# Kernel tuning notes

Measured on AMD Instinct MI355X. Metric: run time of the kernel, lower is better.

Reference implementation:

```python
import jax, jax.numpy as jnp
import numpy as np

N_NODES = 50000
N_EDGES = 600000
D = 128
EPS = 1e-5
AVG_D_LOG = float(np.log(4 + 1))  # avg_d={'log': log(avg_d+1)}, avg_d=4


def setup_inputs() -> dict:
    key = jax.random.key(0)
    ks = jax.random.split(key, 8)
    h = jax.random.normal(ks[0], (N_NODES, D), dtype=jnp.float32)
    # guarantee every node has at least one incoming edge (self-loop)
    edge_dst = jnp.concatenate([
        jnp.arange(N_NODES, dtype=jnp.int64),
        jax.random.randint(ks[1], (N_EDGES - N_NODES,), 0, N_NODES).astype(jnp.int64),
    ])
    edge_src = jax.random.randint(ks[2], (N_EDGES,), 0, N_NODES).astype(jnp.int64)
    def lin(k, fan_in, fan_out):
        lim = 1.0 / np.sqrt(fan_in)
        return jax.random.uniform(k, (fan_in, fan_out), jnp.float32, -lim, lim)
    W_pre = lin(ks[3], 2 * D, D)
    b_pre = jnp.zeros((D,), jnp.float32)
    W_post = lin(ks[4], 12 * D + D, D)  # 4 aggregators * 3 scalers * D + in_dim
    b_post = jnp.zeros((D,), jnp.float32)
    W_mix = lin(ks[5], D, D)
    b_mix = jnp.zeros((D,), jnp.float32)
    return {"h": h, "edge_src": edge_src, "edge_dst": edge_dst,
            "W_pre": W_pre, "b_pre": b_pre, "W_post": W_post,
            "b_post": b_post, "W_mix": W_mix, "b_mix": b_mix}


def reference(h, edge_src, edge_dst, W_pre, b_pre, W_post, b_post, W_mix, b_mix):
    n = h.shape[0]
    # pretrans_edges: cat(src, dst) -> Linear -> ReLU (MLP act) -> ReLU (outer)
    z2 = jnp.concatenate([h[edge_src], h[edge_dst]], axis=1)        # [E, 2D]
    e = jax.nn.relu(z2 @ W_pre + b_pre)                             # [E, D]
    # multi-aggregator segment reduce over destination nodes
    deg = jax.ops.segment_sum(jnp.ones_like(edge_dst, jnp.float32), edge_dst, n)  # [N]
    inv_deg = 1.0 / deg[:, None]
    mean = jax.ops.segment_sum(e, edge_dst, n) * inv_deg
    mean_sq = jax.ops.segment_sum(e * e, edge_dst, n) * inv_deg
    std = jnp.sqrt(jax.nn.relu(mean_sq - mean * mean) + EPS)
    mx = jax.ops.segment_max(e, edge_dst, n)
    mn = jax.ops.segment_min(e, edge_dst, n)
    agg = jnp.concatenate([mean, mx, mn, std], axis=1)              # [N, 4D]
    # scalers: identity, amplification, attenuation
    log_d = jnp.log(deg + 1.0)[:, None]
    scaled = jnp.concatenate([agg, agg * (log_d / AVG_D_LOG), agg * (AVG_D_LOG / log_d)], axis=1)  # [N, 12D]
    # posttrans: cat(h, aggregated) -> Linear -> ReLU
    hp = jax.nn.relu(jnp.concatenate([h, scaled], axis=1) @ W_post + b_post)  # [N, D]
    # mixing network + residual (node_dim == out_dim)
    out = h + jax.nn.leaky_relu(hp @ W_mix + b_mix, negative_slope=0.01)
    return out
```

## Files before the change

### kernel.cpp

```cpp
#include <hip/hip_runtime.h>
#include <hip/hip_bf16.h>

#define N_NODES 50000
#define N_EDGES 600000
#define D 128
#define NB_SCAN 196

constexpr float AVG_D_LOG = 1.6094379124341003f;
constexpr float EPS_V = 1e-5f;

#define PQ_B     0ul
#define AGG_B    25600000ul
#define HBF_B    76800000ul
#define WPRET2_B 89600000ul
#define WPOSTT_B 89665536ul
#define WMIXT_B  90091520ul
#define DEGC_B   90124288ul
#define OFF_B    90324288ul
#define CUR_B    90524352ul
#define SRCS_B   90724352ul
#define BSUM_B   93124352ul

typedef __attribute__((ext_vector_type(8))) short bf16x8;
typedef __attribute__((ext_vector_type(4))) float f32x4;

__device__ __forceinline__ short f2b(float f) {
    unsigned u = __builtin_bit_cast(unsigned, f);
    u += 0x7fffu + ((u >> 16) & 1u);
    return (short)(u >> 16);
}
__device__ __forceinline__ unsigned pk2(float a, float b) {
    return (unsigned)(unsigned short)f2b(a) | ((unsigned)(unsigned short)f2b(b) << 16);
}
__device__ __forceinline__ float blo(unsigned u) { return __uint_as_float(u << 16); }
__device__ __forceinline__ float bhi(unsigned u) { return __uint_as_float(u & 0xffff0000u); }

__device__ __forceinline__ void gld_lds16(const void* g, void* l) {
    __builtin_amdgcn_global_load_lds(
        (const __attribute__((address_space(1))) void*)g,
        (__attribute__((address_space(3))) void*)l, 16, 0, 0);
}

#define WAIT_BAR(N) do {                                              \
    asm volatile("s_waitcnt vmcnt(" #N ")" ::: "memory");             \
    __builtin_amdgcn_sched_barrier(0);                                \
    __builtin_amdgcn_s_barrier();                                     \
    __builtin_amdgcn_sched_barrier(0);                                \
} while (0)
#define BAR_ONLY() do {                                               \
    __builtin_amdgcn_sched_barrier(0);                                \
    __builtin_amdgcn_s_barrier();                                     \
    __builtin_amdgcn_sched_barrier(0);                                \
} while (0)

__global__ __launch_bounds__(256) void prep_kernel(
    const float* __restrict__ h, const float* __restrict__ Wpre,
    const float* __restrict__ Wpost, const float* __restrict__ Wmix,
    short* __restrict__ hbf, short* __restrict__ wpreT2,
    short* __restrict__ wpostT, short* __restrict__ wmixT,
    int* __restrict__ degc, int* __restrict__ cursor)
{
    long i = (long)blockIdx.x * 256 + threadIdx.x;
    if (i < 800000) {
        float4 a = *(const float4*)(h + i * 8);
        float4 b = *(const float4*)(h + i * 8 + 4);
        int4 v;
        v.x = (int)pk2(a.x, a.y); v.y = (int)pk2(a.z, a.w);
        v.z = (int)pk2(b.x, b.y); v.w = (int)pk2(b.z, b.w);
        *(int4*)(hbf + i * 8) = v;
        return;
    }
    i -= 800000;
    if (i < 32768) {
        int n = i >> 7, k = i & 127;
        float v = (n < 128) ? Wpre[k * 128 + n] : Wpre[(k + 128) * 128 + (n - 128)];
        wpreT2[n * 128 + k] = f2b(v);
        return;
    }
    i -= 32768;
    if (i < 212992) { int k = i >> 7, n = i & 127; wpostT[n * 1664 + k] = f2b(Wpost[k * 128 + n]); return; }
    i -= 212992;
    if (i < 16384) { int k = i >> 7, n = i & 127; wmixT[n * 128 + k] = f2b(Wmix[k * 128 + n]); return; }
    i -= 16384;
    if (i < N_NODES) { degc[i] = 0; return; }
    i -= N_NODES;
    if (i < N_NODES) cursor[i] = 0;
}
#define PREP_BLOCKS ((800000 + 32768 + 212992 + 16384 + 2 * N_NODES + 255) / 256)

__global__ __launch_bounds__(256) void hist_kernel(const int* __restrict__ edst, int* __restrict__ degc) {
    int e = blockIdx.x * 256 + threadIdx.x;
    if (e < N_EDGES) atomicAdd(&degc[edst[e]], 1);
}

__global__ __launch_bounds__(256) void scan1_kernel(const int* __restrict__ degc, int* __restrict__ bsum) {
    int n = blockIdx.x * 256 + threadIdx.x;
    int v = (n < N_NODES) ? degc[n] : 0;
#pragma unroll
    for (int o = 32; o > 0; o >>= 1) v += __shfl_down(v, o);
    __shared__ int w4[4];
    if ((threadIdx.x & 63) == 0) w4[threadIdx.x >> 6] = v;
    __syncthreads();
    if (threadIdx.x == 0) bsum[blockIdx.x] = w4[0] + w4[1] + w4[2] + w4[3];
}

__global__ __launch_bounds__(256) void scan2_kernel(int* __restrict__ bsum, int* __restrict__ off) {
    __shared__ int sd[256];
    int tid = threadIdx.x;
    int v = (tid < NB_SCAN) ? bsum[tid] : 0;
    sd[tid] = v;
    __syncthreads();
    for (int o = 1; o < 256; o <<= 1) {
        int t = (tid >= o) ? sd[tid - o] : 0;
        __syncthreads();
        sd[tid] += t;
        __syncthreads();
    }
    if (tid < NB_SCAN) bsum[tid] = sd[tid] - v;
    if (tid == 0) off[N_NODES] = sd[255];
}

__global__ __launch_bounds__(256) void scan3_kernel(const int* __restrict__ degc,
                                                    const int* __restrict__ bsum, int* __restrict__ off) {
    __shared__ int sd[256];
    int tid = threadIdx.x;
    int n = blockIdx.x * 256 + tid;
    int v = (n < N_NODES) ? degc[n] : 0;
    sd[tid] = v;
    __syncthreads();
    for (int o = 1; o < 256; o <<= 1) {
        int t = (tid >= o) ? sd[tid - o] : 0;
        __syncthreads();
        sd[tid] += t;
        __syncthreads();
    }
    if (n < N_NODES) off[n] = sd[tid] - v + bsum[blockIdx.x];
}

__global__ __launch_bounds__(256) void scatter_kernel(const int* __restrict__ esrc, const int* __restrict__ edst,
                                                      const int* __restrict__ off, int* __restrict__ cursor,
                                                      int* __restrict__ srcs) {
    int e = blockIdx.x * 256 + threadIdx.x;
    if (e < N_EDGES) {
        int d = edst[e];
        int p = off[d] + atomicAdd(&cursor[d], 1);
        srcs[p] = esrc[e];
    }
}

__global__ __launch_bounds__(256) void gemm_pq_kernel(
    const short* __restrict__ hbf, const short* __restrict__ wpreT2,
    const float* __restrict__ bpre, short* __restrict__ PQ)
{
    __shared__ __align__(16) short As[128][72];
    __shared__ __align__(16) short Bs[128][72];

    const int tid = threadIdx.x;
    const int cg = blockIdx.x & 1;
    const int bn = (blockIdx.x >> 1) * 128;
    const int lane = tid & 63, wv = tid >> 6;
    const int lm = lane & 15, quad = lane >> 4;

    f32x4 acc[2][8];
#pragma unroll
    for (int a = 0; a < 2; a++)
#pragma unroll
        for (int b = 0; b < 8; b++) acc[a][b] = (f32x4){0.f, 0.f, 0.f, 0.f};

#pragma unroll
    for (int kc = 0; kc < 2; kc++) {
        __syncthreads();
#pragma unroll
        for (int t = 0; t < 4; t++) {
            int q = tid + t * 256;
            int m = q >> 3, seg = q & 7;
            int n = bn + m; if (n >= N_NODES) n = N_NODES - 1;
            *(int4*)&As[m][seg * 8] = *(const int4*)(hbf + (long)n * 128 + kc * 64 + seg * 8);
        }
#pragma unroll
        for (int t = 0; t < 4; t++) {
            int q = tid + t * 256;
            int n = q >> 3, seg = q & 7;
            *(int4*)&Bs[n][seg * 8] = *(const int4*)(wpreT2 + (cg * 128 + n) * 128 + kc * 64 + seg * 8);
        }
        __syncthreads();
#pragma unroll
        for (int ks = 0; ks < 2; ks++) {
            const int ko = ks * 32 + quad * 8;
            bf16x8 a0 = *(const bf16x8*)&As[wv * 32 + lm][ko];
            bf16x8 a1 = *(const bf16x8*)&As[wv * 32 + 16 + lm][ko];
#pragma unroll
            for (int ct = 0; ct < 8; ct++) {
                bf16x8 b = *(const bf16x8*)&Bs[ct * 16 + lm][ko];
                acc[0][ct] = __builtin_amdgcn_mfma_f32_16x16x32_bf16(b, a0, acc[0][ct], 0, 0, 0);
                acc[1][ct] = __builtin_amdgcn_mfma_f32_16x16x32_bf16(b, a1, acc[1][ct], 0, 0, 0);
            }
        }
    }

#pragma unroll
    for (int rt = 0; rt < 2; rt++) {
        int row = wv * 32 + rt * 16 + lm;
        int n = bn + row;
        if (n >= N_NODES) continue;
        short* dst = PQ + (long)n * 256;
#pragma unroll
        for (int ct = 0; ct < 8; ct++) {
            int col = cg * 128 + ct * 16 + quad * 4;
            float v0 = acc[rt][ct][0], v1 = acc[rt][ct][1], v2 = acc[rt][ct][2], v3 = acc[rt][ct][3];
            if (cg) {
                float4 bv = *(const float4*)(bpre + (col - 128));
                v0 += bv.x; v1 += bv.y; v2 += bv.z; v3 += bv.w;
            }
            int2 pkd; pkd.x = (int)pk2(v0, v1); pkd.y = (int)pk2(v2, v3);
            *(int2*)(dst + col) = pkd;
        }
    }
}

__global__ __launch_bounds__(256) void edgestats_kernel(
    const short* __restrict__ PQ, const int* __restrict__ srcs,
    const int* __restrict__ off, short* __restrict__ aggbf)
{
    const int wv = threadIdx.x >> 6, lane = threadIdx.x & 63;
    const int n = blockIdx.x * 4 + wv;
    const unsigned* Pb = (const unsigned*)PQ;

    const int s0 = __builtin_amdgcn_readfirstlane(off[n]);
    const int s1 = __builtin_amdgcn_readfirstlane(off[n + 1]);

    unsigned qu = Pb[(long)n * 128 + 64 + lane];
    const float qa = blo(qu), qb = bhi(qu);

    float sA = 0.f, sB = 0.f, qA = 0.f, qB = 0.f;
    float mxA = -1e30f, mxB = -1e30f, mnA = 1e30f, mnB = 1e30f;

    int p = s0;
    for (; p + 8 <= s1; p += 8) {
        int idx[8];
#pragma unroll
        for (int j = 0; j < 8; j++) idx[j] = srcs[p + j];
        unsigned u[8];
#pragma unroll
        for (int j = 0; j < 8; j++) u[j] = Pb[(long)idx[j] * 128 + lane];
#pragma unroll
        for (int j = 0; j < 8; j++) {
            float a = blo(u[j]) + qa; a = a > 0.f ? a : 0.f;
            float b = bhi(u[j]) + qb; b = b > 0.f ? b : 0.f;
            sA += a; sB += b; qA += a * a; qB += b * b;
            mxA = fmaxf(mxA, a); mxB = fmaxf(mxB, b);
            mnA = fminf(mnA, a); mnB = fminf(mnB, b);
        }
    }
    for (; p < s1; p++) {
        unsigned u = Pb[(long)srcs[p] * 128 + lane];
        float a = blo(u) + qa; a = a > 0.f ? a : 0.f;
        float b = bhi(u) + qb; b = b > 0.f ? b : 0.f;
        sA += a; sB += b; qA += a * a; qB += b * b;
        mxA = fmaxf(mxA, a); mxB = fmaxf(mxB, b);
        mnA = fminf(mnA, a); mnB = fminf(mnB, b);
    }

    float inv = 1.0f / (float)(s1 - s0);
    float mA = sA * inv, mB = sB * inv;
    float vA = qA * inv - mA * mA; vA = vA > 0.f ? vA : 0.f;
    float vB = qB * inv - mB * mB; vB = vB > 0.f ? vB : 0.f;
    float stA = sqrtf(vA + EPS_V), stB = sqrtf(vB + EPS_V);

    unsigned* ag = (unsigned*)(aggbf + (long)n * 512);
    ag[lane]       = pk2(mA, mB);
    ag[64 + lane]  = pk2(mxA, mxB);
    ag[128 + lane] = pk2(mnA, mnB);
    ag[192 + lane] = pk2(stA, stB);
}


__device__ __forceinline__ void stageA_t(short* ldsT, const short* src, int rs, int co,
                                         int bn, int wv, int lane) {
    const int sub = lane >> 3, seg = lane & 7;
    const int sg = (seg ^ sub) * 8;
#pragma unroll
    for (int t = 0; t < 4; t++) {
        int i = wv * 4 + t;
        int row = i * 8 + sub;
        int n = bn + row; if (n >= N_NODES) n = N_NODES - 1;
        gld_lds16(src + (long)n * rs + co + sg, ldsT + i * 512);
    }
}
__device__ __forceinline__ void stageB_t(short* ldsT, const short* src, int rs, int co,
                                         int wv, int lane) {
    const int sub = lane >> 3, seg = lane & 7;
    const int sg = (seg ^ sub) * 8;
#pragma unroll
    for (int t = 0; t < 4; t++) {
        int i = wv * 4 + t;
        int row = i * 8 + sub;
        gld_lds16(src + (long)row * rs + co + sg, ldsT + i * 512);
    }
}

#define MFMA_ITER(AB, BB, ACC)                                                      \
    {                                                                               \
        _Pragma("unroll")                                                           \
        for (int ks = 0; ks < 2; ks++) {                                            \
            const int qx = (((ks * 4 + quad) ^ r7) * 8);                            \
            bf16x8 a0 = *(const bf16x8*)&(AB)[(wv * 32 + lm) * 64 + qx];            \
            bf16x8 a1 = *(const bf16x8*)&(AB)[(wv * 32 + 16 + lm) * 64 + qx];       \
            _Pragma("unroll")                                                       \
            for (int ct = 0; ct < 8; ct++) {                                        \
                bf16x8 b = *(const bf16x8*)&(BB)[(ct * 16 + lm) * 64 + qx];         \
                ACC[0][ct] = __builtin_amdgcn_mfma_f32_16x16x32_bf16(b, a0, ACC[0][ct], 0, 0, 0); \
                ACC[1][ct] = __builtin_amdgcn_mfma_f32_16x16x32_bf16(b, a1, ACC[1][ct], 0, 0, 0); \
            }                                                                       \
        }                                                                           \
    }

__global__ __launch_bounds__(256, 2) void node_kernel(
    const float* __restrict__ h, const short* __restrict__ hbf, const short* __restrict__ aggbf,
    const int* __restrict__ degc, const short* __restrict__ wpostT, const float* __restrict__ bpost,
    const short* __restrict__ wmixT, const float* __restrict__ bmix, float* __restrict__ out)
{
    __shared__ __align__(16) short As[2][8192];
    __shared__ __align__(16) short Bs[2][8192];
    __shared__ float sAmp[128], sAtt[128];

    const int tid = threadIdx.x;
    const int bn = blockIdx.x * 128;
    const int lane = tid & 63, wv = tid >> 6;
    const int lm = lane & 15, quad = lane >> 4;
    const int r7 = lm & 7;

    if (tid < 128) {
        int n = bn + tid; if (n >= N_NODES) n = N_NODES - 1;
        float d = (float)degc[n];
        float ld = logf(d + 1.0f);
        sAmp[tid] = ld * (1.0f / AVG_D_LOG);
        sAtt[tid] = AVG_D_LOG / ld;
    }
    __syncthreads();

    f32x4 accI[2][8], accM[2][8], accT[2][8];
#pragma unroll
    for (int a = 0; a < 2; a++)
#pragma unroll
        for (int b = 0; b < 8; b++) {
            accI[a][b] = (f32x4){0.f, 0.f, 0.f, 0.f};
            accM[a][b] = (f32x4){0.f, 0.f, 0.f, 0.f};
            accT[a][b] = (f32x4){0.f, 0.f, 0.f, 0.f};
        }


    stageA_t(As[0], hbf, 128, 0, bn, wv, lane);
    stageB_t(Bs[0], wpostT, 1664, 0, wv, lane);

    stageA_t(As[1], hbf, 128, 64, bn, wv, lane);
    stageB_t(Bs[1], wpostT, 1664, 64, wv, lane);
    WAIT_BAR(8);
    MFMA_ITER(As[0], Bs[0], accI);
    BAR_ONLY();

    stageB_t(Bs[0], wpostT, 1664, 2 * 64, wv, lane);
    stageA_t(As[0], aggbf, 512, 0, bn, wv, lane);
    WAIT_BAR(8);
    MFMA_ITER(As[1], Bs[1], accI);
    BAR_ONLY();

    int pb = 0;
    for (int j = 0; j < 8; j++) {
        short* Ac = As[j & 1];
        stageB_t(Bs[pb ^ 1], wpostT, 1664, (10 + j) * 64, wv, lane);
        if (j < 7) {
            int jn = j + 1;
            stageA_t(As[jn & 1], aggbf, 512, (jn >> 1) * 128 + (jn & 1) * 64, bn, wv, lane);
            WAIT_BAR(8);
        } else {
            WAIT_BAR(4);
        }
        MFMA_ITER(Ac, Bs[pb], accI);
        BAR_ONLY();

        stageB_t(Bs[pb], wpostT, 1664, (18 + j) * 64, wv, lane);
        if (j < 7) { WAIT_BAR(8); } else { WAIT_BAR(4); }
        MFMA_ITER(Ac, Bs[pb ^ 1], accM);
        BAR_ONLY();

        if (j < 7) stageB_t(Bs[pb ^ 1], wpostT, 1664, (3 + j) * 64, wv, lane);
        else       stageB_t(Bs[pb ^ 1], wmixT, 128, 0, wv, lane);
        WAIT_BAR(4);
        MFMA_ITER(Ac, Bs[pb], accT);
        BAR_ONLY();
        pb ^= 1;
    }

    stageB_t(Bs[1], wmixT, 128, 64, wv, lane);

    const float am0 = sAmp[wv * 32 + lm],      at0 = sAtt[wv * 32 + lm];
    const float am1 = sAmp[wv * 32 + 16 + lm], at1 = sAtt[wv * 32 + 16 + lm];
#pragma unroll
    for (int rt = 0; rt < 2; rt++) {
        const float am = rt ? am1 : am0, at = rt ? at1 : at0;
        const int row = wv * 32 + rt * 16 + lm;
#pragma unroll
        for (int ct = 0; ct < 8; ct++) {
            float4 bv = *(const float4*)(bpost + ct * 16 + quad * 4);
            float v0 = accI[rt][ct][0] + am * accM[rt][ct][0] + at * accT[rt][ct][0] + bv.x;
            float v1 = accI[rt][ct][1] + am * accM[rt][ct][1] + at * accT[rt][ct][1] + bv.y;
            float v2 = accI[rt][ct][2] + am * accM[rt][ct][2] + at * accT[rt][ct][2] + bv.z;
            float v3 = accI[rt][ct][3] + am * accM[rt][ct][3] + at * accT[rt][ct][3] + bv.w;
            v0 = v0 > 0.f ? v0 : 0.f; v1 = v1 > 0.f ? v1 : 0.f;
            v2 = v2 > 0.f ? v2 : 0.f; v3 = v3 > 0.f ? v3 : 0.f;
            int2 pkd; pkd.x = (int)pk2(v0, v1); pkd.y = (int)pk2(v2, v3);
            const int cb = (ct & 3) * 32 + quad * 8;
            const int sb = ((((cb >> 4) ^ r7) << 4) | (cb & 15));
            *(int2*)((char*)As[ct >> 2] + row * 128 + sb) = pkd;
        }
    }
    __syncthreads();

    f32x4 accO[2][8];
#pragma unroll
    for (int a = 0; a < 2; a++)
#pragma unroll
        for (int b = 0; b < 8; b++) accO[a][b] = (f32x4){0.f, 0.f, 0.f, 0.f};
#pragma unroll
    for (int kc = 0; kc < 2; kc++) {
        MFMA_ITER(As[kc], Bs[kc], accO);
    }

#pragma unroll
    for (int rt = 0; rt < 2; rt++) {
        int row = wv * 32 + rt * 16 + lm;
        int n = bn + row;
        if (n >= N_NODES) continue;
#pragma unroll
        for (int ct = 0; ct < 8; ct++) {
            int col = ct * 16 + quad * 4;
            float4 bv = *(const float4*)(bmix + col);
            float4 hv = *(const float4*)(h + (long)n * 128 + col);
            float4 o;
            float v0 = accO[rt][ct][0] + bv.x; v0 = v0 > 0.f ? v0 : 0.01f * v0; o.x = hv.x + v0;
            float v1 = accO[rt][ct][1] + bv.y; v1 = v1 > 0.f ? v1 : 0.01f * v1; o.y = hv.y + v1;
            float v2 = accO[rt][ct][2] + bv.z; v2 = v2 > 0.f ? v2 : 0.01f * v2; o.z = hv.z + v2;
            float v3 = accO[rt][ct][3] + bv.w; v3 = v3 > 0.f ? v3 : 0.01f * v3; o.w = hv.w + v3;
            *(float4*)(out + (long)n * 128 + col) = o;
        }
    }
}

extern "C" void kernel_launch(void* const* d_in, const int* in_sizes, int n_in,
                              void* d_out, int out_size, void* d_ws, size_t ws_size,
                              hipStream_t stream) {
    const float* h     = (const float*)d_in[0];
    const int*   esrc  = (const int*)d_in[1];
    const int*   edst  = (const int*)d_in[2];
    const float* Wpre  = (const float*)d_in[3];
    const float* bpre  = (const float*)d_in[4];
    const float* Wpost = (const float*)d_in[5];
    const float* bpost = (const float*)d_in[6];
    const float* Wmix  = (const float*)d_in[7];
    const float* bmix  = (const float*)d_in[8];
    float* out = (float*)d_out;
    char* ws = (char*)d_ws;

    short* PQ     = (short*)(ws + PQ_B);
    short* aggbf  = (short*)(ws + AGG_B);
    short* hbf    = (short*)(ws + HBF_B);
    short* wpreT2 = (short*)(ws + WPRET2_B);
    short* wpostT = (short*)(ws + WPOSTT_B);
    short* wmixT  = (short*)(ws + WMIXT_B);
    int*   degc   = (int*)(ws + DEGC_B);
    int*   off    = (int*)(ws + OFF_B);
    int*   cursor = (int*)(ws + CUR_B);
    int*   srcs   = (int*)(ws + SRCS_B);
    int*   bsum   = (int*)(ws + BSUM_B);

    prep_kernel<<<PREP_BLOCKS, 256, 0, stream>>>(h, Wpre, Wpost, Wmix, hbf, wpreT2, wpostT, wmixT, degc, cursor);
    hist_kernel<<<(N_EDGES + 255) / 256, 256, 0, stream>>>(edst, degc);
    scan1_kernel<<<NB_SCAN, 256, 0, stream>>>(degc, bsum);
    scan2_kernel<<<1, 256, 0, stream>>>(bsum, off);
    scan3_kernel<<<NB_SCAN, 256, 0, stream>>>(degc, bsum, off);
    scatter_kernel<<<(N_EDGES + 255) / 256, 256, 0, stream>>>(esrc, edst, off, cursor, srcs);
    gemm_pq_kernel<<<((N_NODES + 127) / 128) * 2, 256, 0, stream>>>(hbf, wpreT2, bpre, PQ);
    edgestats_kernel<<<N_NODES / 4, 256, 0, stream>>>(PQ, srcs, off, aggbf);
    node_kernel<<<(N_NODES + 127) / 128, 256, 0, stream>>>(h, hbf, aggbf, degc, wpostT, bpost, wmixT, bmix, out);
}
```

Baseline: 259.9 us.

## Halve node_kernel row tile and fold scaler accumulators into one

The node kernel now processes 64 nodes per block instead of 128, with the four waves split into a 2x2 row/column grid so each wave owns a 32x64 output tile. The separate identity, amplification and attenuation accumulators are merged: each scaled partial product is computed into a temporary and immediately folded into the main accumulator with the per-node scaler. This roughly cuts accumulator registers and LDS per block, allowing three blocks per CU and about twice as many blocks. The cost is that every block re-streams the full weight matrix for half as many rows, plus extra FMA work per k-step.

```diff
diff --git a/kernel.cpp b/kernel.cpp
--- a/kernel.cpp
+++ b/kernel.cpp
@@ -280,8 +280,8 @@
     const int sub = lane >> 3, seg = lane & 7;
     const int sg = (seg ^ sub) * 8;
 #pragma unroll
-    for (int t = 0; t < 4; t++) {
-        int i = wv * 4 + t;
+    for (int t = 0; t < 2; t++) {
+        int i = wv * 2 + t;
         int row = i * 8 + sub;
         int n = bn + row; if (n >= N_NODES) n = N_NODES - 1;
         gld_lds16(src + (long)n * rs + co + sg, ldsT + i * 512);
@@ -299,38 +299,41 @@
     }
 }
 
-#define MFMA_ITER(AB, BB, ACC)                                                      \
+#define MFMA_GROUP(AB, BB, ACC, FRESH)                                              \
     {                                                                               \
         _Pragma("unroll")                                                           \
         for (int ks = 0; ks < 2; ks++) {                                            \
             const int qx = (((ks * 4 + quad) ^ r7) * 8);                            \
-            bf16x8 a0 = *(const bf16x8*)&(AB)[(wv * 32 + lm) * 64 + qx];            \
-            bf16x8 a1 = *(const bf16x8*)&(AB)[(wv * 32 + 16 + lm) * 64 + qx];       \
+            bf16x8 a0 = *(const bf16x8*)&(AB)[(rg * 32 + lm) * 64 + qx];            \
+            bf16x8 a1 = *(const bf16x8*)&(AB)[(rg * 32 + 16 + lm) * 64 + qx];       \
             _Pragma("unroll")                                                       \
-            for (int ct = 0; ct < 8; ct++) {                                        \
-                bf16x8 b = *(const bf16x8*)&(BB)[(ct * 16 + lm) * 64 + qx];         \
-                ACC[0][ct] = __builtin_amdgcn_mfma_f32_16x16x32_bf16(b, a0, ACC[0][ct], 0, 0, 0); \
-                ACC[1][ct] = __builtin_amdgcn_mfma_f32_16x16x32_bf16(b, a1, ACC[1][ct], 0, 0, 0); \
+            for (int ct = 0; ct < 4; ct++) {                                        \
+                bf16x8 b = *(const bf16x8*)&(BB)[(cg * 64 + ct * 16 + lm) * 64 + qx]; \
+                f32x4 c0 = ((FRESH) && ks == 0) ? (f32x4){0.f,0.f,0.f,0.f} : ACC[0][ct]; \
+                f32x4 c1 = ((FRESH) && ks == 0) ? (f32x4){0.f,0.f,0.f,0.f} : ACC[1][ct]; \
+                ACC[0][ct] = __builtin_amdgcn_mfma_f32_16x16x32_bf16(b, a0, c0, 0, 0, 0); \
+                ACC[1][ct] = __builtin_amdgcn_mfma_f32_16x16x32_bf16(b, a1, c1, 0, 0, 0); \
             }                                                                       \
         }                                                                           \
     }
 
-__global__ __launch_bounds__(256, 2) void node_kernel(
+__global__ __launch_bounds__(256, 3) void node_kernel(
     const float* __restrict__ h, const short* __restrict__ hbf, const short* __restrict__ aggbf,
     const int* __restrict__ degc, const short* __restrict__ wpostT, const float* __restrict__ bpost,
     const short* __restrict__ wmixT, const float* __restrict__ bmix, float* __restrict__ out)
 {
-    __shared__ __align__(16) short As[2][8192];
+    __shared__ __align__(16) short As[2][4096];
     __shared__ __align__(16) short Bs[2][8192];
-    __shared__ float sAmp[128], sAtt[128];
+    __shared__ float sAmp[64], sAtt[64];
 
     const int tid = threadIdx.x;
-    const int bn = blockIdx.x * 128;
+    const int bn = blockIdx.x * 64;
     const int lane = tid & 63, wv = tid >> 6;
+    const int rg = wv & 1, cg = wv >> 1;
     const int lm = lane & 15, quad = lane >> 4;
     const int r7 = lm & 7;
 
-    if (tid < 128) {
+    if (tid < 64) {
         int n = bn + tid; if (n >= N_NODES) n = N_NODES - 1;
         float d = (float)degc[n];
         float ld = logf(d + 1.0f);
@@ -339,15 +342,11 @@
     }
     __syncthreads();
 
-    f32x4 accI[2][8], accM[2][8], accT[2][8];
-#pragma unroll
-    for (int a = 0; a < 2; a++)
-#pragma unroll
-        for (int b = 0; b < 8; b++) {
-            accI[a][b] = (f32x4){0.f, 0.f, 0.f, 0.f};
-            accM[a][b] = (f32x4){0.f, 0.f, 0.f, 0.f};
-            accT[a][b] = (f32x4){0.f, 0.f, 0.f, 0.f};
-        }
+    const float am0 = sAmp[rg * 32 + lm],      at0 = sAtt[rg * 32 + lm];
+    const float am1 = sAmp[rg * 32 + 16 + lm], at1 = sAtt[rg * 32 + 16 + lm];
+
+    f32x4 mI[2][4];
+    f32x4 tmpA[2][4];
 
 
     stageA_t(As[0], hbf, 128, 0, bn, wv, lane);
@@ -355,86 +354,86 @@
 
     stageA_t(As[1], hbf, 128, 64, bn, wv, lane);
     stageB_t(Bs[1], wpostT, 1664, 64, wv, lane);
-    WAIT_BAR(8);
-    MFMA_ITER(As[0], Bs[0], accI);
+    WAIT_BAR(6);
+    MFMA_GROUP(As[0], Bs[0], mI, 1);
     BAR_ONLY();
 
     stageB_t(Bs[0], wpostT, 1664, 2 * 64, wv, lane);
     stageA_t(As[0], aggbf, 512, 0, bn, wv, lane);
-    WAIT_BAR(8);
-    MFMA_ITER(As[1], Bs[1], accI);
+    WAIT_BAR(6);
+    MFMA_GROUP(As[1], Bs[1], mI, 0);
     BAR_ONLY();
 
     int pb = 0;
     for (int j = 0; j < 8; j++) {
-        short* Ac = As[j & 1];
+        const short* Ac = As[j & 1];
         stageB_t(Bs[pb ^ 1], wpostT, 1664, (10 + j) * 64, wv, lane);
         if (j < 7) {
             int jn = j + 1;
             stageA_t(As[jn & 1], aggbf, 512, (jn >> 1) * 128 + (jn & 1) * 64, bn, wv, lane);
-            WAIT_BAR(8);
+            WAIT_BAR(6);
         } else {
             WAIT_BAR(4);
         }
-        MFMA_ITER(Ac, Bs[pb], accI);
+        MFMA_GROUP(Ac, Bs[pb], mI, 0);
         BAR_ONLY();
 
         stageB_t(Bs[pb], wpostT, 1664, (18 + j) * 64, wv, lane);
-        if (j < 7) { WAIT_BAR(8); } else { WAIT_BAR(4); }
-        MFMA_ITER(Ac, Bs[pb ^ 1], accM);
+        if (j < 7) { WAIT_BAR(6); } else { WAIT_BAR(4); }
+        MFMA_GROUP(Ac, Bs[pb ^ 1], tmpA, 1);
+#pragma unroll
+        for (int ct = 0; ct < 4; ct++) {
+            mI[0][ct] += am0 * tmpA[0][ct];
+            mI[1][ct] += am1 * tmpA[1][ct];
+        }
         BAR_ONLY();
 
         if (j < 7) stageB_t(Bs[pb ^ 1], wpostT, 1664, (3 + j) * 64, wv, lane);
         else       stageB_t(Bs[pb ^ 1], wmixT, 128, 0, wv, lane);
         WAIT_BAR(4);
-        MFMA_ITER(Ac, Bs[pb], accT);
+        MFMA_GROUP(Ac, Bs[pb], tmpA, 1);
+#pragma unroll
+        for (int ct = 0; ct < 4; ct++) {
+            mI[0][ct] += at0 * tmpA[0][ct];
+            mI[1][ct] += at1 * tmpA[1][ct];
+        }
         BAR_ONLY();
         pb ^= 1;
     }
 
     stageB_t(Bs[1], wmixT, 128, 64, wv, lane);
-
-    const float am0 = sAmp[wv * 32 + lm],      at0 = sAtt[wv * 32 + lm];
-    const float am1 = sAmp[wv * 32 + 16 + lm], at1 = sAtt[wv * 32 + 16 + lm];
 #pragma unroll
     for (int rt = 0; rt < 2; rt++) {
-        const float am = rt ? am1 : am0, at = rt ? at1 : at0;
-        const int row = wv * 32 + rt * 16 + lm;
-#pragma unroll
-        for (int ct = 0; ct < 8; ct++) {
-            float4 bv = *(const float4*)(bpost + ct * 16 + quad * 4);
-            float v0 = accI[rt][ct][0] + am * accM[rt][ct][0] + at * accT[rt][ct][0] + bv.x;
-            float v1 = accI[rt][ct][1] + am * accM[rt][ct][1] + at * accT[rt][ct][1] + bv.y;
-            float v2 = accI[rt][ct][2] + am * accM[rt][ct][2] + at * accT[rt][ct][2] + bv.z;
-            float v3 = accI[rt][ct][3] + am * accM[rt][ct][3] + at * accT[rt][ct][3] + bv.w;
-            v0 = v0 > 0.f ? v0 : 0.f; v1 = v1 > 0.f ? v1 : 0.f;
-            v2 = v2 > 0.f ? v2 : 0.f; v3 = v3 > 0.f ? v3 : 0.f;
+        const int row = rg * 32 + rt * 16 + lm;
+#pragma unroll
+        for (int ct = 0; ct < 4; ct++) {
+            float4 bv = *(const float4*)(bpost + cg * 64 + ct * 16 + quad * 4);
+            float v0 = mI[rt][ct][0] + bv.x; v0 = v0 > 0.f ? v0 : 0.f;
+            float v1 = mI[rt][ct][1] + bv.y; v1 = v1 > 0.f ? v1 : 0.f;
+            float v2 = mI[rt][ct][2] + bv.z; v2 = v2 > 0.f ? v2 : 0.f;
+            float v3 = mI[rt][ct][3] + bv.w; v3 = v3 > 0.f ? v3 : 0.f;
             int2 pkd; pkd.x = (int)pk2(v0, v1); pkd.y = (int)pk2(v2, v3);
-            const int cb = (ct & 3) * 32 + quad * 8;
+            const int cb = ct * 32 + quad * 8;
             const int sb = ((((cb >> 4) ^ r7) << 4) | (cb & 15));
-            *(int2*)((char*)As[ct >> 2] + row * 128 + sb) = pkd;
+            *(int2*)((char*)As[cg] + row * 128 + sb) = pkd;
         }
     }
     __syncthreads();
 
-    f32x4 accO[2][8];
-#pragma unroll
-    for (int a = 0; a < 2; a++)
-#pragma unroll
-        for (int b = 0; b < 8; b++) accO[a][b] = (f32x4){0.f, 0.f, 0.f, 0.f};
+    f32x4 accO[2][4];
 #pragma unroll
     for (int kc = 0; kc < 2; kc++) {
-        MFMA_ITER(As[kc], Bs[kc], accO);
+        MFMA_GROUP(As[kc], Bs[kc], accO, kc == 0);
     }
 
 #pragma unroll
     for (int rt = 0; rt < 2; rt++) {
-        int row = wv * 32 + rt * 16 + lm;
+        int row = rg * 32 + rt * 16 + lm;
         int n = bn + row;
         if (n >= N_NODES) continue;
 #pragma unroll
-        for (int ct = 0; ct < 8; ct++) {
-            int col = ct * 16 + quad * 4;
+        for (int ct = 0; ct < 4; ct++) {
+            int col = cg * 64 + ct * 16 + quad * 4;
             float4 bv = *(const float4*)(bmix + col);
             float4 hv = *(const float4*)(h + (long)n * 128 + col);
             float4 o;
@@ -482,5 +481,5 @@
     scatter_kernel<<<(N_EDGES + 255) / 256, 256, 0, stream>>>(esrc, edst, off, cursor, srcs);
     gemm_pq_kernel<<<((N_NODES + 127) / 128) * 2, 256, 0, stream>>>(hbf, wpreT2, bpre, PQ);
     edgestats_kernel<<<N_NODES / 4, 256, 0, stream>>>(PQ, srcs, off, aggbf);
-    node_kernel<<<(N_NODES + 127) / 128, 256, 0, stream>>>(h, hbf, aggbf, degc, wpostT, bpost, wmixT, bmix, out);
-}
+    node_kernel<<<(N_NODES + 63) / 64, 256, 0, stream>>>(h, hbf, aggbf, degc, wpostT, bpost, wmixT, bmix, out);
+}
```

Measured after the change: 265.7 us. 2.2% more time.

## Restructure node GEMM: 64-row blocks, register A fragments, single accumulator with scaler folding

Applied to the files above, without the earlier changes.

The node kernel now processes 64 nodes per block with 128 threads. A fragments are loaded directly from global memory into registers instead of being staged through LDS. The three accumulator sets (identity, amplification, attenuation) are merged into one: amp/att partials go into temporary tiles that are scaled and added after each chunk, which cuts accumulator register pressure. MFMA sections are also wrapped with s_setprio. The aim is higher occupancy and less LDS traffic, at the cost of more blocks and weight tiles being restaged per 64 rows instead of per 128.

```diff
diff --git a/kernel.cpp b/kernel.cpp
--- a/kernel.cpp
+++ b/kernel.cpp
@@ -275,62 +275,88 @@
 }
 
 
-__device__ __forceinline__ void stageA_t(short* ldsT, const short* src, int rs, int co,
-                                         int bn, int wv, int lane) {
+__device__ __forceinline__ void stageB(short* ldsT, const short* src, int rs, int co,
+                                       int wv, int lane) {
     const int sub = lane >> 3, seg = lane & 7;
     const int sg = (seg ^ sub) * 8;
 #pragma unroll
-    for (int t = 0; t < 4; t++) {
-        int i = wv * 4 + t;
-        int row = i * 8 + sub;
-        int n = bn + row; if (n >= N_NODES) n = N_NODES - 1;
-        gld_lds16(src + (long)n * rs + co + sg, ldsT + i * 512);
-    }
-}
-__device__ __forceinline__ void stageB_t(short* ldsT, const short* src, int rs, int co,
-                                         int wv, int lane) {
-    const int sub = lane >> 3, seg = lane & 7;
-    const int sg = (seg ^ sub) * 8;
-#pragma unroll
-    for (int t = 0; t < 4; t++) {
-        int i = wv * 4 + t;
+    for (int t = 0; t < 8; t++) {
+        int i = wv * 8 + t;
         int row = i * 8 + sub;
         gld_lds16(src + (long)row * rs + co + sg, ldsT + i * 512);
     }
 }
 
-#define MFMA_ITER(AB, BB, ACC)                                                      \
+__device__ __forceinline__ void loadA(bf16x8* a, const short* src, int rs, int co,
+                                      int bn, int wv, int lm, int quad) {
+#pragma unroll
+    for (int rt = 0; rt < 2; rt++)
+#pragma unroll
+        for (int ks = 0; ks < 2; ks++) {
+            int n = bn + wv * 32 + rt * 16 + lm; if (n >= N_NODES) n = N_NODES - 1;
+            a[rt * 2 + ks] = *(const bf16x8*)(src + (long)n * rs + co + ks * 32 + quad * 8);
+        }
+}
+
+#define GROUP_ID(BB, AF)                                                            \
     {                                                                               \
+        __builtin_amdgcn_s_setprio(1);                                              \
         _Pragma("unroll")                                                           \
         for (int ks = 0; ks < 2; ks++) {                                            \
-            const int qx = (((ks * 4 + quad) ^ r7) * 8);                            \
-            bf16x8 a0 = *(const bf16x8*)&(AB)[(wv * 32 + lm) * 64 + qx];            \
-            bf16x8 a1 = *(const bf16x8*)&(AB)[(wv * 32 + 16 + lm) * 64 + qx];       \
+            const int qx = ((ks * 4 + quad) ^ r7) * 8;                              \
             _Pragma("unroll")                                                       \
             for (int ct = 0; ct < 8; ct++) {                                        \
                 bf16x8 b = *(const bf16x8*)&(BB)[(ct * 16 + lm) * 64 + qx];         \
-                ACC[0][ct] = __builtin_amdgcn_mfma_f32_16x16x32_bf16(b, a0, ACC[0][ct], 0, 0, 0); \
-                ACC[1][ct] = __builtin_amdgcn_mfma_f32_16x16x32_bf16(b, a1, ACC[1][ct], 0, 0, 0); \
+                mI[0][ct] = __builtin_amdgcn_mfma_f32_16x16x32_bf16(b, (AF)[ks], mI[0][ct], 0, 0, 0); \
+                mI[1][ct] = __builtin_amdgcn_mfma_f32_16x16x32_bf16(b, (AF)[2 + ks], mI[1][ct], 0, 0, 0); \
             }                                                                       \
         }                                                                           \
-    }
-
-__global__ __launch_bounds__(256, 2) void node_kernel(
+        __builtin_amdgcn_s_setprio(0);                                              \
+    }
+
+#define GROUP_SC(BB, AF, S0, S1)                                                    \
+    {                                                                               \
+        _Pragma("unroll")                                                           \
+        for (int ch = 0; ch < 2; ch++) {                                            \
+            f32x4 tp[2][4];                                                         \
+            __builtin_amdgcn_s_setprio(1);                                          \
+            _Pragma("unroll")                                                       \
+            for (int ks = 0; ks < 2; ks++) {                                        \
+                const int qx = ((ks * 4 + quad) ^ r7) * 8;                          \
+                _Pragma("unroll")                                                   \
+                for (int c = 0; c < 4; c++) {                                       \
+                    bf16x8 b = *(const bf16x8*)&(BB)[((ch * 4 + c) * 16 + lm) * 64 + qx]; \
+                    f32x4 c0 = ks ? tp[0][c] : (f32x4){0.f, 0.f, 0.f, 0.f};         \
+                    f32x4 c1 = ks ? tp[1][c] : (f32x4){0.f, 0.f, 0.f, 0.f};         \
+                    tp[0][c] = __builtin_amdgcn_mfma_f32_16x16x32_bf16(b, (AF)[ks], c0, 0, 0, 0); \
+                    tp[1][c] = __builtin_amdgcn_mfma_f32_16x16x32_bf16(b, (AF)[2 + ks], c1, 0, 0, 0); \
+                }                                                                   \
+            }                                                                       \
+            __builtin_amdgcn_s_setprio(0);                                          \
+            _Pragma("unroll")                                                       \
+            for (int c = 0; c < 4; c++) {                                           \
+                mI[0][ch * 4 + c] += (S0) * tp[0][c];                               \
+                mI[1][ch * 4 + c] += (S1) * tp[1][c];                               \
+            }                                                                       \
+        }                                                                           \
+    }
+
+__global__ __launch_bounds__(128, 2) void node_kernel(
     const float* __restrict__ h, const short* __restrict__ hbf, const short* __restrict__ aggbf,
     const int* __restrict__ degc, const short* __restrict__ wpostT, const float* __restrict__ bpost,
     const short* __restrict__ wmixT, const float* __restrict__ bmix, float* __restrict__ out)
 {
-    __shared__ __align__(16) short As[2][8192];
     __shared__ __align__(16) short Bs[2][8192];
-    __shared__ float sAmp[128], sAtt[128];
+    __shared__ __align__(16) short AsH[2][4096];
+    __shared__ float sAmp[64], sAtt[64];
 
     const int tid = threadIdx.x;
-    const int bn = blockIdx.x * 128;
+    const int bn = blockIdx.x * 64;
     const int lane = tid & 63, wv = tid >> 6;
     const int lm = lane & 15, quad = lane >> 4;
     const int r7 = lm & 7;
 
-    if (tid < 128) {
+    if (tid < 64) {
         int n = bn + tid; if (n >= N_NODES) n = N_NODES - 1;
         float d = (float)degc[n];
         float ld = logf(d + 1.0f);
@@ -339,92 +365,92 @@
     }
     __syncthreads();
 
-    f32x4 accI[2][8], accM[2][8], accT[2][8];
-#pragma unroll
-    for (int a = 0; a < 2; a++)
-#pragma unroll
-        for (int b = 0; b < 8; b++) {
-            accI[a][b] = (f32x4){0.f, 0.f, 0.f, 0.f};
-            accM[a][b] = (f32x4){0.f, 0.f, 0.f, 0.f};
-            accT[a][b] = (f32x4){0.f, 0.f, 0.f, 0.f};
-        }
-
-
-    stageA_t(As[0], hbf, 128, 0, bn, wv, lane);
-    stageB_t(Bs[0], wpostT, 1664, 0, wv, lane);
-
-    stageA_t(As[1], hbf, 128, 64, bn, wv, lane);
-    stageB_t(Bs[1], wpostT, 1664, 64, wv, lane);
-    WAIT_BAR(8);
-    MFMA_ITER(As[0], Bs[0], accI);
-    BAR_ONLY();
-
-    stageB_t(Bs[0], wpostT, 1664, 2 * 64, wv, lane);
-    stageA_t(As[0], aggbf, 512, 0, bn, wv, lane);
-    WAIT_BAR(8);
-    MFMA_ITER(As[1], Bs[1], accI);
-    BAR_ONLY();
-
-    int pb = 0;
-    for (int j = 0; j < 8; j++) {
-        short* Ac = As[j & 1];
-        stageB_t(Bs[pb ^ 1], wpostT, 1664, (10 + j) * 64, wv, lane);
-        if (j < 7) {
-            int jn = j + 1;
-            stageA_t(As[jn & 1], aggbf, 512, (jn >> 1) * 128 + (jn & 1) * 64, bn, wv, lane);
-            WAIT_BAR(8);
-        } else {
-            WAIT_BAR(4);
-        }
-        MFMA_ITER(Ac, Bs[pb], accI);
-        BAR_ONLY();
-
-        stageB_t(Bs[pb], wpostT, 1664, (18 + j) * 64, wv, lane);
-        if (j < 7) { WAIT_BAR(8); } else { WAIT_BAR(4); }
-        MFMA_ITER(Ac, Bs[pb ^ 1], accM);
-        BAR_ONLY();
-
-        if (j < 7) stageB_t(Bs[pb ^ 1], wpostT, 1664, (3 + j) * 64, wv, lane);
-        else       stageB_t(Bs[pb ^ 1], wmixT, 128, 0, wv, lane);
-        WAIT_BAR(4);
-        MFMA_ITER(Ac, Bs[pb], accT);
-        BAR_ONLY();
-        pb ^= 1;
-    }
-
-    stageB_t(Bs[1], wmixT, 128, 64, wv, lane);
-
     const float am0 = sAmp[wv * 32 + lm],      at0 = sAtt[wv * 32 + lm];
     const float am1 = sAmp[wv * 32 + 16 + lm], at1 = sAtt[wv * 32 + 16 + lm];
+
+    f32x4 mI[2][8];
+    bf16x8 aF[2][4];
+
+    loadA(aF[0], hbf, 128, 0, bn, wv, lm, quad);
+    loadA(aF[1], hbf, 128, 64, bn, wv, lm, quad);
+    stageB(Bs[0], wpostT, 1664, 0, wv, lane);
+
+#pragma unroll
+    for (int a = 0; a < 2; a++)
+#pragma unroll
+        for (int b = 0; b < 8; b++) mI[a][b] = (f32x4){0.f, 0.f, 0.f, 0.f};
+    stageB(Bs[1], wpostT, 1664, 64, wv, lane);
+    WAIT_BAR(8);
+    GROUP_ID(Bs[0], aF[0]);
+    BAR_ONLY();
+
+    stageB(Bs[0], wpostT, 1664, 2 * 64, wv, lane);
+    loadA(aF[0], aggbf, 512, 0, bn, wv, lm, quad);
+    WAIT_BAR(12);
+    GROUP_ID(Bs[1], aF[1]);
+    BAR_ONLY();
+
+#pragma unroll
+    for (int j = 0; j < 8; j++) {
+        const int pb = j & 1;
+        stageB(Bs[pb ^ 1], wpostT, 1664, (10 + j) * 64, wv, lane);
+        WAIT_BAR(8);
+        GROUP_ID(Bs[pb], aF[j & 1]);
+        BAR_ONLY();
+
+        stageB(Bs[pb], wpostT, 1664, (18 + j) * 64, wv, lane);
+        WAIT_BAR(8);
+        GROUP_SC(Bs[pb ^ 1], aF[j & 1], am0, am1);
+        BAR_ONLY();
+
+        if (j < 7) {
+            stageB(Bs[pb ^ 1], wpostT, 1664, (3 + j) * 64, wv, lane);
+            loadA(aF[(j + 1) & 1], aggbf, 512, ((j + 1) >> 1) * 128 + ((j + 1) & 1) * 64, bn, wv, lm, quad);
+            WAIT_BAR(12);
+        } else {
+            stageB(Bs[pb ^ 1], wmixT, 128, 0, wv, lane);
+            WAIT_BAR(8);
+        }
+        GROUP_SC(Bs[pb], aF[j & 1], at0, at1);
+        BAR_ONLY();
+    }
+
+    stageB(Bs[1], wmixT, 128, 64, wv, lane);
 #pragma unroll
     for (int rt = 0; rt < 2; rt++) {
-        const float am = rt ? am1 : am0, at = rt ? at1 : at0;
         const int row = wv * 32 + rt * 16 + lm;
 #pragma unroll
         for (int ct = 0; ct < 8; ct++) {
             float4 bv = *(const float4*)(bpost + ct * 16 + quad * 4);
-            float v0 = accI[rt][ct][0] + am * accM[rt][ct][0] + at * accT[rt][ct][0] + bv.x;
-            float v1 = accI[rt][ct][1] + am * accM[rt][ct][1] + at * accT[rt][ct][1] + bv.y;
-            float v2 = accI[rt][ct][2] + am * accM[rt][ct][2] + at * accT[rt][ct][2] + bv.z;
-            float v3 = accI[rt][ct][3] + am * accM[rt][ct][3] + at * accT[rt][ct][3] + bv.w;
-            v0 = v0 > 0.f ? v0 : 0.f; v1 = v1 > 0.f ? v1 : 0.f;
-            v2 = v2 > 0.f ? v2 : 0.f; v3 = v3 > 0.f ? v3 : 0.f;
+            float v0 = mI[rt][ct][0] + bv.x; v0 = v0 > 0.f ? v0 : 0.f;
+            float v1 = mI[rt][ct][1] + bv.y; v1 = v1 > 0.f ? v1 : 0.f;
+            float v2 = mI[rt][ct][2] + bv.z; v2 = v2 > 0.f ? v2 : 0.f;
+            float v3 = mI[rt][ct][3] + bv.w; v3 = v3 > 0.f ? v3 : 0.f;
             int2 pkd; pkd.x = (int)pk2(v0, v1); pkd.y = (int)pk2(v2, v3);
             const int cb = (ct & 3) * 32 + quad * 8;
             const int sb = ((((cb >> 4) ^ r7) << 4) | (cb & 15));
-            *(int2*)((char*)As[ct >> 2] + row * 128 + sb) = pkd;
+            *(int2*)((char*)AsH[ct >> 2] + row * 128 + sb) = pkd;
         }
     }
     __syncthreads();
 
     f32x4 accO[2][8];
 #pragma unroll
-    for (int a = 0; a < 2; a++)
-#pragma unroll
-        for (int b = 0; b < 8; b++) accO[a][b] = (f32x4){0.f, 0.f, 0.f, 0.f};
-#pragma unroll
     for (int kc = 0; kc < 2; kc++) {
-        MFMA_ITER(As[kc], Bs[kc], accO);
+#pragma unroll
+        for (int ks = 0; ks < 2; ks++) {
+            const int qx = ((ks * 4 + quad) ^ r7) * 8;
+            bf16x8 a0 = *(const bf16x8*)&AsH[kc][(wv * 32 + lm) * 64 + qx];
+            bf16x8 a1 = *(const bf16x8*)&AsH[kc][(wv * 32 + 16 + lm) * 64 + qx];
+#pragma unroll
+            for (int ct = 0; ct < 8; ct++) {
+                bf16x8 b = *(const bf16x8*)&Bs[kc][(ct * 16 + lm) * 64 + qx];
+                f32x4 c0 = (kc == 0 && ks == 0) ? (f32x4){0.f, 0.f, 0.f, 0.f} : accO[0][ct];
+                f32x4 c1 = (kc == 0 && ks == 0) ? (f32x4){0.f, 0.f, 0.f, 0.f} : accO[1][ct];
+                accO[0][ct] = __builtin_amdgcn_mfma_f32_16x16x32_bf16(b, a0, c0, 0, 0, 0);
+                accO[1][ct] = __builtin_amdgcn_mfma_f32_16x16x32_bf16(b, a1, c1, 0, 0, 0);
+            }
+        }
     }
 
 #pragma unroll
@@ -482,5 +508,5 @@
     scatter_kernel<<<(N_EDGES + 255) / 256, 256, 0, stream>>>(esrc, edst, off, cursor, srcs);
     gemm_pq_kernel<<<((N_NODES + 127) / 128) * 2, 256, 0, stream>>>(hbf, wpreT2, bpre, PQ);
     edgestats_kernel<<<N_NODES / 4, 256, 0, stream>>>(PQ, srcs, off, aggbf);
-    node_kernel<<<(N_NODES + 127) / 128, 256, 0, stream>>>(h, hbf, aggbf, degc, wpostT, bpost, wmixT, bmix, out);
-}
+    node_kernel<<<(N_NODES + 63) / 64, 128, 0, stream>>>(h, hbf, aggbf, degc, wpostT, bpost, wmixT, bmix, out);
+}
```

Result: slower. 273.4 us (+5.2%).
